# Kernel tuning notes

Hardware: AMD Instinct MI355X
Metric: run time of the kernel (lower is better)

The kernel has to match this reference:

```python
import jax, jax.numpy as jnp
import numpy as np

MARGIN = 1.0
EPS = 1e-10


def setup_inputs() -> dict:
    key = jax.random.key(0)
    k1, k2, k3 = jax.random.split(key, 3)
    C, D = 4096, 1024
    B, A = 8, 32
    cls_features = jax.random.normal(k1, (C, D), dtype=jnp.float32)
    prototypes = jax.random.normal(k2, (C, D), dtype=jnp.float32)
    annotations = jax.random.randint(k3, (B, A, 5), 0, C, dtype=jnp.int64)
    return {"cls_features": cls_features, "prototypes": prototypes,
            "annotations": annotations, "steps": 1000}


def reference(cls_features, prototypes, annotations, steps):
    C, D = cls_features.shape
    protos = jax.lax.stop_gradient(prototypes)  # prototypes.detach()

    # one_hot presence of each class in the batch annotations (col 4 = class id, -1 = pad)
    targets = annotations[:, :, 4]                      # [B, A]
    valid = targets != -1
    counts = jnp.zeros((C,), jnp.float32).at[
        jnp.where(valid, targets, 0).ravel()
    ].add(valid.astype(jnp.float32).ravel())
    mask_i = counts > 0                                  # class present in batch
    mask_j = jnp.sum(protos, axis=-1) != 0               # prototypes[j].sum() != 0

    # pairwise mean squared distance: msd[i, j] = mean((feat_i - proto_j)^2)
    f2 = jnp.sum(cls_features * cls_features, axis=-1)   # [C]
    p2 = jnp.sum(protos * protos, axis=-1)               # [C]
    cross = cls_features @ protos.T                      # [C, C]
    msd = jnp.maximum(f2[:, None] + p2[None, :] - 2.0 * cross, 0.0) / D

    pair_mask = mask_i[:, None] & mask_j[None, :]
    eye = jnp.eye(C, dtype=bool)
    intra_mask = pair_mask & eye
    inter_mask = pair_mask & ~eye

    intra_count = jnp.sum(intra_mask.astype(jnp.float32))
    inter_count = jnp.sum(inter_mask.astype(jnp.float32))

    intra_loss = jnp.sum(jnp.where(intra_mask, msd, 0.0)) / (intra_count + EPS)

    s = jnp.sqrt(jnp.maximum(msd, 1e-12))
    e = MARGIN - s
    inter_term = (e / MARGIN) ** 2 * jnp.maximum(e, 0.0) ** 2
    inter_loss = jnp.sum(jnp.where(inter_mask, inter_term, 0.0)) / (inter_count + EPS)

    return (intra_loss, inter_loss)
```

## Files before the change

### kernel.cpp

```cpp
#include <hip/hip_runtime.h>
#include <hip/hip_bf16.h>

typedef float f32x4 __attribute__((ext_vector_type(4)));
typedef int   i32x4 __attribute__((ext_vector_type(4)));
typedef int   i32x8 __attribute__((ext_vector_type(8)));

#define NC 4096
#define ND 1024
#define NVP 256
#define EPSF 1e-10f
#define SCALE1 127
#define NBLK2 256


__global__ __launch_bounds__(256)
void fprep_kernel(const int* __restrict__ ann, int n_ann,
                  const float* __restrict__ F,
                  unsigned char* __restrict__ Fc, float* __restrict__ f2c,
                  int* __restrict__ vidx, int* __restrict__ nv,
                  float* __restrict__ accum, int* __restrict__ ticket) {
  __shared__ unsigned char mark[NC];
  __shared__ int wsum[4];
  __shared__ int vloc[NVP];
  __shared__ float rs[4];
  const int tid = threadIdx.x;
  const int lane = tid & 63, wid = tid >> 6;

  for (int i = tid; i < NC; i += 256) mark[i] = 0;
  __syncthreads();
  for (int t = tid; t < n_ann; t += 256) {
    int idx = ann[t * 5 + 4];
    if (idx >= 0 && idx < NC) mark[idx] = 1;
  }
  __syncthreads();
  int base = tid * 16, lc = 0;
  #pragma unroll
  for (int k = 0; k < 16; ++k) lc += mark[base + k];
  int inc = lc;
  #pragma unroll
  for (int off = 1; off < 64; off <<= 1) {
    int v = __shfl_up(inc, off);
    if (lane >= off) inc += v;
  }
  if (lane == 63) wsum[wid] = inc;
  __syncthreads();
  int wbase = 0;
  for (int w = 0; w < wid; ++w) wbase += wsum[w];
  int pos = wbase + inc - lc;
  for (int k = 0; k < 16; ++k)
    if (mark[base + k]) vloc[pos++] = base + k;
  const int total = wsum[0] + wsum[1] + wsum[2] + wsum[3];
  __syncthreads();

  if (blockIdx.x == 0) {
    for (int i = tid; i < NVP; i += 256) vidx[i] = (i < total) ? vloc[i] : 0;
    if (tid == 0) *nv = total;
    if (tid < 8) accum[tid] = 0.f;
    if (tid == 8) *ticket = 0;
  }

  const int slot = blockIdx.x;
  if (slot >= total) return;
  const int row = vloc[slot];
  float4 v = *reinterpret_cast<const float4*>(F + (size_t)row * ND + tid * 4);
  int pk = __builtin_amdgcn_cvt_pk_fp8_f32(v.x, v.y, 0, false);
  pk = __builtin_amdgcn_cvt_pk_fp8_f32(v.z, v.w, pk, true);
  {
    int d0 = tid * 4;
    int kt = d0 >> 7, hif = (d0 >> 5) & 3, half = (d0 >> 4) & 1, b = d0 & 15;
    int R16 = slot >> 4, lof = slot & 15;
    size_t fa = ((((size_t)kt * 16 + R16) * 2 + half) * 64 + hif * 16 + lof) * 16 + b;
    *reinterpret_cast<int*>(Fc + fa) = pk;
  }
  float sq = v.x * v.x + v.y * v.y + v.z * v.z + v.w * v.w;
  #pragma unroll
  for (int off = 32; off; off >>= 1) sq += __shfl_down(sq, off);
  if (lane == 0) rs[wid] = sq;
  __syncthreads();
  if (tid == 0) f2c[slot] = rs[0] + rs[1] + rs[2] + rs[3];
}

#define LDFRAG(V, BASEPTR, FID)                                               \
  do {                                                                        \
    const unsigned char* _p = (BASEPTR) + (size_t)(FID) * 2048 + lane * 16;   \
    i32x4 _l0 = *(const i32x4*)(_p);                                          \
    i32x4 _l1 = *(const i32x4*)(_p + 1024);                                   \
    V = __builtin_shufflevector(_l0, _l1, 0, 1, 2, 3, 4, 5, 6, 7);            \
  } while (0)

__global__ __launch_bounds__(512)
void pgemm_kernel(const float* __restrict__ P,
                  const unsigned char* __restrict__ Fc,
                  const float* __restrict__ f2c,
                  const int* __restrict__ vidx, const int* __restrict__ nv,
                  float* __restrict__ accum, int* __restrict__ ticket,
                  float* __restrict__ out) {
  __shared__ __attribute__((aligned(16))) unsigned char bfrag[8 * 2048];
  __shared__ float p2l[16], psl[16], redI[8], redE[8], redN[8];
  const int tid = threadIdx.x;
  const int lane = tid & 63, wid = tid >> 6;
  const int bj = blockIdx.x;
  const int total = *nv;

  {
    const int r = tid >> 5;
    const int seg = tid & 31;
    const float* src = P + (size_t)(bj * 16 + r) * ND;
    float sq = 0.f, sm = 0.f;
    #pragma unroll
    for (int i = 0; i < 8; ++i) {
      float4 v = *reinterpret_cast<const float4*>(src + (seg + i * 32) * 4);
      int pk = __builtin_amdgcn_cvt_pk_fp8_f32(v.x, v.y, 0, false);
      pk = __builtin_amdgcn_cvt_pk_fp8_f32(v.z, v.w, pk, true);
      int addr = i * 2048 + r * 128 + ((seg * 4) ^ ((r & 7) << 4));
      *reinterpret_cast<int*>(&bfrag[addr]) = pk;
      sq += v.x * v.x + v.y * v.y + v.z * v.z + v.w * v.w;
      sm += v.x + v.y + v.z + v.w;
    }
    #pragma unroll
    for (int off = 16; off; off >>= 1) {
      sq += __shfl_down(sq, off, 32);
      sm += __shfl_down(sm, off, 32);
    }
    if ((tid & 31) == 0) { p2l[r] = sq; psl[r] = sm; }
  }
  __syncthreads();

  const int lo = lane & 15, hi = lane >> 4;
  f32x4 acc0 = {0.f, 0.f, 0.f, 0.f}, acc1 = acc0;
  const int fbase = wid * 2;
  #pragma unroll 4
  for (int kt = 0; kt < 8; ++kt) {
    i32x8 a0, a1, b;
    LDFRAG(a0, Fc, kt * 16 + fbase);
    LDFRAG(a1, Fc, kt * 16 + fbase + 1);
    {
      int x = (lo & 7) << 4;
      const unsigned char* bb = &bfrag[kt * 2048 + lo * 128];
      i32x4 l0 = *reinterpret_cast<const i32x4*>(bb + ((hi * 32) ^ x));
      i32x4 l1 = *reinterpret_cast<const i32x4*>(bb + ((hi * 32 + 16) ^ x));
      b = __builtin_shufflevector(l0, l1, 0, 1, 2, 3, 4, 5, 6, 7);
    }
    acc0 = __builtin_amdgcn_mfma_scale_f32_16x16x128_f8f6f4(
        a0, b, acc0, 0, 0, 0, SCALE1, 0, SCALE1);
    acc1 = __builtin_amdgcn_mfma_scale_f32_16x16x128_f8f6f4(
        a1, b, acc1, 0, 0, 0, SCALE1, 0, SCALE1);
  }

  float intra_l = 0.f, inter_l = 0.f;
  {
    const int gj = bj * 16 + lo;
    const float p2j = p2l[lo];
    const bool mj = psl[lo] != 0.f;
    if (mj) {
      #pragma unroll
      for (int f = 0; f < 2; ++f) {
        f32x4 a = f ? acc1 : acc0;
        #pragma unroll
        for (int r = 0; r < 4; ++r) {
          int ci = wid * 32 + f * 16 + hi * 4 + r;
          if (ci < total) {
            float msd = fmaxf(f2c[ci] + p2j - 2.f * a[r], 0.f) * (1.f / 1024.f);
            int gi = vidx[ci];
            if (gi == gj) {
              intra_l += msd;
            } else if (msd < 1.0f) {
              float s = sqrtf(fmaxf(msd, 1e-12f));
              float e = 1.f - s;
              float e2 = e * e;
              inter_l += e2 * e2;
            }
          }
        }
      }
    }
  }
  float ndl = 0.f;
  for (int c = tid; c < total; c += 512) {
    int v = vidx[c];
    if ((v >> 4) == bj && psl[v & 15] != 0.f) ndl += 1.f;
  }
  #pragma unroll
  for (int off = 32; off; off >>= 1) {
    intra_l += __shfl_down(intra_l, off);
    inter_l += __shfl_down(inter_l, off);
    ndl     += __shfl_down(ndl, off);
  }
  if (lane == 0) { redI[wid] = intra_l; redE[wid] = inter_l; redN[wid] = ndl; }
  __syncthreads();

  if (tid == 0) {
    float si = 0.f, se = 0.f, nd = 0.f;
    #pragma unroll
    for (int w = 0; w < 8; ++w) { si += redI[w]; se += redE[w]; nd += redN[w]; }
    float nj = 0.f;
    #pragma unroll
    for (int r = 0; r < 16; ++r) nj += (psl[r] != 0.f) ? 1.f : 0.f;
    atomicAdd(&accum[0], si);
    atomicAdd(&accum[1], se);
    atomicAdd(&accum[2], nj);
    atomicAdd(&accum[3], nd);
    asm volatile("s_waitcnt vmcnt(0)" ::: "memory");
    int tkt = atomicAdd(ticket, 1);
    if (tkt == NBLK2 - 1) {
      float a0 = atomicAdd(&accum[0], 0.f);
      float a1 = atomicAdd(&accum[1], 0.f);
      float fnj = atomicAdd(&accum[2], 0.f);
      float fnd = atomicAdd(&accum[3], 0.f);
      float fni = (float)total;
      out[0] = a0 / (fnd + EPSF);
      out[1] = a1 / (fni * fnj - fnd + EPSF);
    }
  }
}

extern "C" void kernel_launch(void* const* d_in, const int* in_sizes, int n_in,
                              void* d_out, int out_size, void* d_ws, size_t ws_size,
                              hipStream_t stream) {
  const float* F = (const float*)d_in[0];
  const float* P = (const float*)d_in[1];
  const int* ann = (const int*)d_in[2];
  int n_ann = in_sizes[2] / 5;

  char* ws = (char*)d_ws;
  unsigned char* Fc = (unsigned char*)ws;
  float* f2c    = (float*)(ws + (size_t)NVP * ND);
  float* accum  = f2c + NVP;
  int*   vidx   = (int*)(accum + 8);
  int*   nv     = vidx + NVP;
  int*   ticket = nv + 1;

  float* out = (float*)d_out;

  fprep_kernel<<<NVP, 256, 0, stream>>>(ann, n_ann, F, Fc, f2c, vidx, nv, accum, ticket);
  pgemm_kernel<<<NBLK2, 512, 0, stream>>>(P, Fc, f2c, vidx, nv, accum, ticket, out);
}
```

Measured before the change: 32.94 us.

## Fuse feature prep into GEMM kernel, recomputing FP8 features per block in LDS

Removes the separate feature-prep kernel and its global FP8 staging buffer. Each GEMM block now rebuilds the class-presence list from annotations itself, then loads the valid feature rows from global memory, quantizes them to FP8 into shared memory, and computes row norms per k-tile. A tiny zero kernel resets the accumulators. This trades one launch and a global round trip for redundant per-block work: every one of the 256 blocks rescans annotations and reloads the same 256 feature rows, and two extra barriers are added per k iteration.

```diff
diff --git a/kernel.cpp b/kernel.cpp
--- a/kernel.cpp
+++ b/kernel.cpp
@@ -10,74 +10,13 @@
 #define NVP 256
 #define EPSF 1e-10f
 #define SCALE1 127
-#define NBLK2 256
-
-
-__global__ __launch_bounds__(256)
-void fprep_kernel(const int* __restrict__ ann, int n_ann,
-                  const float* __restrict__ F,
-                  unsigned char* __restrict__ Fc, float* __restrict__ f2c,
-                  int* __restrict__ vidx, int* __restrict__ nv,
-                  float* __restrict__ accum, int* __restrict__ ticket) {
-  __shared__ unsigned char mark[NC];
-  __shared__ int wsum[4];
-  __shared__ int vloc[NVP];
-  __shared__ float rs[4];
-  const int tid = threadIdx.x;
-  const int lane = tid & 63, wid = tid >> 6;
-
-  for (int i = tid; i < NC; i += 256) mark[i] = 0;
-  __syncthreads();
-  for (int t = tid; t < n_ann; t += 256) {
-    int idx = ann[t * 5 + 4];
-    if (idx >= 0 && idx < NC) mark[idx] = 1;
-  }
-  __syncthreads();
-  int base = tid * 16, lc = 0;
-  #pragma unroll
-  for (int k = 0; k < 16; ++k) lc += mark[base + k];
-  int inc = lc;
-  #pragma unroll
-  for (int off = 1; off < 64; off <<= 1) {
-    int v = __shfl_up(inc, off);
-    if (lane >= off) inc += v;
-  }
-  if (lane == 63) wsum[wid] = inc;
-  __syncthreads();
-  int wbase = 0;
-  for (int w = 0; w < wid; ++w) wbase += wsum[w];
-  int pos = wbase + inc - lc;
-  for (int k = 0; k < 16; ++k)
-    if (mark[base + k]) vloc[pos++] = base + k;
-  const int total = wsum[0] + wsum[1] + wsum[2] + wsum[3];
-  __syncthreads();
-
-  if (blockIdx.x == 0) {
-    for (int i = tid; i < NVP; i += 256) vidx[i] = (i < total) ? vloc[i] : 0;
-    if (tid == 0) *nv = total;
-    if (tid < 8) accum[tid] = 0.f;
-    if (tid == 8) *ticket = 0;
-  }
-
-  const int slot = blockIdx.x;
-  if (slot >= total) return;
-  const int row = vloc[slot];
-  float4 v = *reinterpret_cast<const float4*>(F + (size_t)row * ND + tid * 4);
-  int pk = __builtin_amdgcn_cvt_pk_fp8_f32(v.x, v.y, 0, false);
-  pk = __builtin_amdgcn_cvt_pk_fp8_f32(v.z, v.w, pk, true);
-  {
-    int d0 = tid * 4;
-    int kt = d0 >> 7, hif = (d0 >> 5) & 3, half = (d0 >> 4) & 1, b = d0 & 15;
-    int R16 = slot >> 4, lof = slot & 15;
-    size_t fa = ((((size_t)kt * 16 + R16) * 2 + half) * 64 + hif * 16 + lof) * 16 + b;
-    *reinterpret_cast<int*>(Fc + fa) = pk;
-  }
-  float sq = v.x * v.x + v.y * v.y + v.z * v.z + v.w * v.w;
-  #pragma unroll
-  for (int off = 32; off; off >>= 1) sq += __shfl_down(sq, off);
-  if (lane == 0) rs[wid] = sq;
-  __syncthreads();
-  if (tid == 0) f2c[slot] = rs[0] + rs[1] + rs[2] + rs[3];
+#define NBLK 256
+
+
+__global__ void zero_kernel(float* __restrict__ accum, int* __restrict__ ticket) {
+  int t = threadIdx.x;
+  if (t < 8) accum[t] = 0.f;
+  if (t == 8) *ticket = 0;
 }
 
 #define LDFRAG(V, BASEPTR, FID)                                               \
@@ -89,18 +28,55 @@
   } while (0)
 
 __global__ __launch_bounds__(512)
-void pgemm_kernel(const float* __restrict__ P,
-                  const unsigned char* __restrict__ Fc,
-                  const float* __restrict__ f2c,
-                  const int* __restrict__ vidx, const int* __restrict__ nv,
+void fused_kernel(const int* __restrict__ ann, int n_ann,
+                  const float* __restrict__ F, const float* __restrict__ P,
                   float* __restrict__ accum, int* __restrict__ ticket,
                   float* __restrict__ out) {
+  __shared__ unsigned char mark[NC];
+  __shared__ int vloc[NVP];
+  __shared__ int wsum[8];
   __shared__ __attribute__((aligned(16))) unsigned char bfrag[8 * 2048];
+  __shared__ __attribute__((aligned(16))) unsigned char afrag[16 * 2048];
+  __shared__ float f2loc[NVP];
   __shared__ float p2l[16], psl[16], redI[8], redE[8], redN[8];
   const int tid = threadIdx.x;
   const int lane = tid & 63, wid = tid >> 6;
   const int bj = blockIdx.x;
-  const int total = *nv;
+
+  for (int i = tid; i < NC; i += 512) mark[i] = 0;
+  __syncthreads();
+  for (int t = tid; t < n_ann; t += 512) {
+    int idx = ann[t * 5 + 4];
+    if (idx >= 0 && idx < NC) mark[idx] = 1;
+  }
+  __syncthreads();
+  int lc = 0;
+  {
+    int base = tid * 8;
+    #pragma unroll
+    for (int k = 0; k < 8; ++k) lc += mark[base + k];
+  }
+  int inc = lc;
+  #pragma unroll
+  for (int off = 1; off < 64; off <<= 1) {
+    int v = __shfl_up(inc, off);
+    if (lane >= off) inc += v;
+  }
+  if (lane == 63) wsum[wid] = inc;
+  __syncthreads();
+  int wbase = 0;
+  for (int w = 0; w < wid; ++w) wbase += wsum[w];
+  int pos = wbase + inc - lc;
+  {
+    int base = tid * 8;
+    for (int k = 0; k < 8; ++k)
+      if (mark[base + k]) vloc[pos++] = base + k;
+  }
+  const int total = wsum[0] + wsum[1] + wsum[2] + wsum[3] +
+                    wsum[4] + wsum[5] + wsum[6] + wsum[7];
+  __syncthreads();
+  for (int i = total + tid; i < NVP; i += 512) vloc[i] = 0;
+  __syncthreads();
 
   {
     const int r = tid >> 5;
@@ -124,16 +100,38 @@
     }
     if ((tid & 31) == 0) { p2l[r] = sq; psl[r] = sm; }
   }
-  __syncthreads();
 
   const int lo = lane & 15, hi = lane >> 4;
+  const int ci = tid >> 1;
+  const int hk = tid & 1;
+  const int prow = vloc[ci];
+  const float* fbase = F + (size_t)prow * ND + hk * 64;
+  unsigned char* adst = &afrag[(ci >> 4) * 2048 + (ci & 15) * 16];
   f32x4 acc0 = {0.f, 0.f, 0.f, 0.f}, acc1 = acc0;
-  const int fbase = wid * 2;
-  #pragma unroll 4
+  const int fbA = wid * 2;
+  #pragma unroll 1
   for (int kt = 0; kt < 8; ++kt) {
+    __syncthreads();
+    {
+      float sq = 0.f;
+      const float* fsrc = fbase + kt * 128;
+      #pragma unroll
+      for (int j = 0; j < 16; ++j) {
+        float4 v = *reinterpret_cast<const float4*>(fsrc + j * 4);
+        int pk = __builtin_amdgcn_cvt_pk_fp8_f32(v.x, v.y, 0, false);
+        pk = __builtin_amdgcn_cvt_pk_fp8_f32(v.z, v.w, pk, true);
+        int kh = hk * 64 + j * 4;
+        *reinterpret_cast<int*>(adst + ((kh >> 4) & 1) * 1024 +
+                                (kh >> 5) * 256 + (kh & 15)) = pk;
+        sq += v.x * v.x + v.y * v.y + v.z * v.z + v.w * v.w;
+      }
+      sq += __shfl_xor(sq, 1);
+      if (hk == 0) f2loc[ci] = (kt == 0) ? sq : (f2loc[ci] + sq);
+    }
+    __syncthreads();
     i32x8 a0, a1, b;
-    LDFRAG(a0, Fc, kt * 16 + fbase);
-    LDFRAG(a1, Fc, kt * 16 + fbase + 1);
+    LDFRAG(a0, afrag, fbA);
+    LDFRAG(a1, afrag, fbA + 1);
     {
       int x = (lo & 7) << 4;
       const unsigned char* bb = &bfrag[kt * 2048 + lo * 128];
@@ -158,10 +156,10 @@
         f32x4 a = f ? acc1 : acc0;
         #pragma unroll
         for (int r = 0; r < 4; ++r) {
-          int ci = wid * 32 + f * 16 + hi * 4 + r;
-          if (ci < total) {
-            float msd = fmaxf(f2c[ci] + p2j - 2.f * a[r], 0.f) * (1.f / 1024.f);
-            int gi = vidx[ci];
+          int cc = wid * 32 + f * 16 + hi * 4 + r;
+          if (cc < total) {
+            float msd = fmaxf(f2loc[cc] + p2j - 2.f * a[r], 0.f) * (1.f / 1024.f);
+            int gi = vloc[cc];
             if (gi == gj) {
               intra_l += msd;
             } else if (msd < 1.0f) {
@@ -177,7 +175,7 @@
   }
   float ndl = 0.f;
   for (int c = tid; c < total; c += 512) {
-    int v = vidx[c];
+    int v = vloc[c];
     if ((v >> 4) == bj && psl[v & 15] != 0.f) ndl += 1.f;
   }
   #pragma unroll
@@ -202,7 +200,7 @@
     atomicAdd(&accum[3], nd);
     asm volatile("s_waitcnt vmcnt(0)" ::: "memory");
     int tkt = atomicAdd(ticket, 1);
-    if (tkt == NBLK2 - 1) {
+    if (tkt == NBLK - 1) {
       float a0 = atomicAdd(&accum[0], 0.f);
       float a1 = atomicAdd(&accum[1], 0.f);
       float fnj = atomicAdd(&accum[2], 0.f);
@@ -223,15 +221,11 @@
   int n_ann = in_sizes[2] / 5;
 
   char* ws = (char*)d_ws;
-  unsigned char* Fc = (unsigned char*)ws;
-  float* f2c    = (float*)(ws + (size_t)NVP * ND);
-  float* accum  = f2c + NVP;
-  int*   vidx   = (int*)(accum + 8);
-  int*   nv     = vidx + NVP;
-  int*   ticket = nv + 1;
+  float* accum  = (float*)ws;
+  int*   ticket = (int*)(accum + 8);
 
   float* out = (float*)d_out;
 
-  fprep_kernel<<<NVP, 256, 0, stream>>>(ann, n_ann, F, Fc, f2c, vidx, nv, accum, ticket);
-  pgemm_kernel<<<NBLK2, 512, 0, stream>>>(P, Fc, f2c, vidx, nv, accum, ticket, out);
+  zero_kernel<<<1, 64, 0, stream>>>(accum, ticket);
+  fused_kernel<<<NBLK, 512, 0, stream>>>(ann, n_ann, F, P, accum, ticket, out);
 }
```

Measured after the change: 65.98 us. +100.3%, slower.
